# Kernel tuning notes

Hardware: AMD Instinct MI355X
Metric: run time of the kernel (lower is better)

## Reference

```python
import jax, jax.numpy as jnp
import numpy as np

B, T, C, HR = 8, 4096, 256, 4
N_LAYER, LAYER_ID = 12, 3
HID = HR * C


def _fancy_decay_first():
    # Faithful reproduction of VRWKV_SpatialMix._init_weights(init_mode='fancy')
    r01 = LAYER_ID / (N_LAYER - 1)
    h = np.arange(C, dtype=np.float32)
    decay = -5.0 + 8.0 * (h / (C - 1)) ** (0.7 + 1.3 * r01)
    zig = ((np.arange(1, C + 1) % 3) - 1).astype(np.float32) * 0.5
    first = np.float32(np.log(0.3)) + zig
    return jnp.asarray(decay, jnp.float32), jnp.asarray(first, jnp.float32)


def setup_inputs() -> dict:
    key = jax.random.key(0)
    ks = jax.random.split(key, 12)
    s = 0.02  # small weight scale keeps exp(k) well-conditioned
    decay, first = _fancy_decay_first()
    return {
        "x": jax.random.normal(ks[0], (B, T, C), jnp.float32),
        "Wk": jax.random.normal(ks[1], (C, C), jnp.float32) * s,
        "Wv": jax.random.normal(ks[2], (C, C), jnp.float32) * s,
        "Wr": jax.random.normal(ks[3], (C, C), jnp.float32) * s,
        "Wo": jax.random.normal(ks[4], (C, C), jnp.float32) * s,
        "Wk_ffn": jax.random.normal(ks[5], (C, HID), jnp.float32) * s,
        "Wv_ffn": jax.random.normal(ks[6], (HID, C), jnp.float32) * s,
        "Wr_ffn": jax.random.normal(ks[7], (C, C), jnp.float32) * s,
        "g1": 1.0 + 0.1 * jax.random.normal(ks[8], (C,), jnp.float32),
        "b1": 0.1 * jax.random.normal(ks[9], (C,), jnp.float32),
        "g2": 1.0 + 0.1 * jax.random.normal(ks[10], (C,), jnp.float32),
        "b2": 0.1 * jax.random.normal(ks[11], (C,), jnp.float32),
        "spatial_decay": decay,
        "spatial_first": first,
    }


def _ln(x, g, b):
    m = jnp.mean(x, axis=-1, keepdims=True)
    v = jnp.var(x, axis=-1, keepdims=True)
    return (x - m) * jax.lax.rsqrt(v + 1e-5) * g + b


def _wkv(w, u, k, v):
    # Numerically-stable log-space WKV recurrence (same math as wkv_cuda):
    # y_t = (sum_{i<t} e^{w*(t-1-i)+k_i} v_i + e^{u+k_t} v_t)
    #     / (sum_{i<t} e^{w*(t-1-i)+k_i}     + e^{u+k_t})
    # w,u: [C]; k,v: [B,T,C] -> y: [B,T,C]
    Bb, Tt, Cc = k.shape
    kT = jnp.swapaxes(k, 0, 1)  # [T,B,C]
    vT = jnp.swapaxes(v, 0, 1)

    def step(carry, kv):
        p, q, o = carry           # [B,C] num / den / running max exponent
        kt, vt = kv               # [B,C]
        no = jnp.maximum(o, u + kt)
        A = jnp.exp(o - no)
        E = jnp.exp(u + kt - no)
        y = (A * p + E * vt) / (A * q + E)
        no2 = jnp.maximum(w + o, kt)
        A2 = jnp.exp(w + o - no2)
        E2 = jnp.exp(kt - no2)
        return (A2 * p + E2 * vt, A2 * q + E2, no2), y

    init = (jnp.zeros((Bb, Cc), k.dtype),
            jnp.zeros((Bb, Cc), k.dtype),
            jnp.full((Bb, Cc), -1e38, k.dtype))
    _, yT = jax.lax.scan(step, init, (kT, vT))
    return jnp.swapaxes(yT, 0, 1)


def reference(x, Wk, Wv, Wr, Wo, Wk_ffn, Wv_ffn, Wr_ffn, g1, b1, g2, b2,
              spatial_decay, spatial_first):
    Tlen = x.shape[1]
    # --- SpatialMix (shift_pixel=0 -> xk=xv=xr=h, key_norm=False) ---
    h = _ln(x, g1, b1)
    k = h @ Wk
    v = h @ Wv
    sr = jax.nn.sigmoid(h @ Wr)
    y = _wkv(spatial_decay / Tlen, spatial_first / Tlen, k, v)
    x = x + (sr * y) @ Wo
    # --- ChannelMix (square-ReLU MLP, sigmoid receptance gate) ---
    h2 = _ln(x, g2, b2)
    kk = jnp.square(jax.nn.relu(h2 @ Wk_ffn))
    x = x + jax.nn.sigmoid(h2 @ Wr_ffn) * (kk @ Wv_ffn)
    return x
```

## Files before the change

### kernel.cpp

```cpp
#include <hip/hip_runtime.h>
#include <hip/hip_bf16.h>
#include <math.h>

#define TDIM 4096
#define CDIM 256
#define BDIM 8
#define NTOK (BDIM * TDIM)
#define HIDDIM 1024
#define NCHUNK 128
#define CHLEN 32

typedef float f32x4 __attribute__((ext_vector_type(4)));
typedef __bf16 bf16x8 __attribute__((ext_vector_type(8)));
typedef __bf16 bf16x4 __attribute__((ext_vector_type(4)));

#define GLDS16(gp, lp) __builtin_amdgcn_global_load_lds( \
    (const __attribute__((address_space(1))) void*)(gp), \
    (__attribute__((address_space(3))) void*)(lp), 16, 0, 0)

#define WAITCNT_VM4 0x0F74
#define WAITCNT_VM3 0x0F73
#define WAITCNT_VM0 0x0F70

__device__ __forceinline__ float sigm(float v) { return 1.0f / (1.0f + __expf(-v)); }

__global__ __launch_bounds__(256) void pack_weights(
    const float* __restrict__ Wk, const float* __restrict__ Wv,
    const float* __restrict__ Wr, const float* __restrict__ Wo,
    const float* __restrict__ Wkf, const float* __restrict__ Wvf,
    const float* __restrict__ Wrf,
    __bf16* __restrict__ WkvrT, __bf16* __restrict__ WoT,
    __bf16* __restrict__ Wkfr, __bf16* __restrict__ WvfT) {
  long long j = (long long)blockIdx.x * 256 + threadIdx.x;
  if (j < 196608) {
    int n = (int)(j >> 8), k = (int)(j & 255);
    const float* src = (n < 256) ? Wk : (n < 512 ? Wv : Wr);
    WkvrT[j] = (__bf16)src[k * 256 + (n & 255)];
    return;
  }
  j -= 196608;
  if (j < 65536) { int n = (int)(j >> 8), k = (int)(j & 255);
    WoT[j] = (__bf16)Wo[k * 256 + n]; return; }
  j -= 65536;
  if (j < 327680) { int n = (int)(j >> 8), k = (int)(j & 255);
    Wkfr[j] = (__bf16)(n < 1024 ? Wkf[(long long)k * 1024 + n]
                                : Wrf[k * 256 + (n - 1024)]);
    return; }
  j -= 327680;
  if (j < 262144) { int n = (int)(j >> 10), k = (int)(j & 1023);
    WvfT[j] = (__bf16)Wvf[(long long)k * 256 + n]; return; }
}

template <typename T>
__global__ __launch_bounds__(256) void ln_kernel(
    const T* __restrict__ x, const float* __restrict__ gamma,
    const float* __restrict__ beta, __bf16* __restrict__ h) {
  const int wave = threadIdx.x >> 6, lane = threadIdx.x & 63;
  const long long row = (long long)blockIdx.x * 4 + wave;
  const long long base = row * CDIM + lane * 4;
  f32x4 v;
  if constexpr (sizeof(T) == 4) {
    v = *(const f32x4*)&x[base];
  } else {
    bf16x4 t = *(const bf16x4*)&x[base];
    v[0] = (float)t[0]; v[1] = (float)t[1]; v[2] = (float)t[2]; v[3] = (float)t[3];
  }
  float s = v[0] + v[1] + v[2] + v[3];
  float s2 = v[0]*v[0] + v[1]*v[1] + v[2]*v[2] + v[3]*v[3];
  #pragma unroll
  for (int o = 1; o < 64; o <<= 1) { s += __shfl_xor(s, o); s2 += __shfl_xor(s2, o); }
  const float mean = s * (1.0f / CDIM);
  const float var = s2 * (1.0f / CDIM) - mean * mean;
  const float rstd = rsqrtf(var + 1e-5f);
  const f32x4 g4 = *(const f32x4*)&gamma[lane * 4];
  const f32x4 b4 = *(const f32x4*)&beta[lane * 4];
  bf16x4 o;
  #pragma unroll
  for (int r = 0; r < 4; r++) o[r] = (__bf16)((v[r] - mean) * rstd * g4[r] + b4[r]);
  *(bf16x4*)&h[base] = o;
}

template <int BN, int EPI>
__global__ __launch_bounds__(256, 5) void gemm4(
    const __bf16* __restrict__ A, const __bf16* __restrict__ Bt,
    int M, int N, int K,
    float* __restrict__ outF, __bf16* __restrict__ outH,
    __bf16* __restrict__ outH2,
    const float* __restrict__ srcF, const __bf16* __restrict__ srcH,
    const __bf16* __restrict__ gate) {
  constexpr int WNT = BN / 32;
  constexpr int NBC = BN / 64;
  __shared__ __bf16 sA[2][128 * 32];
  __shared__ __bf16 sB[2][BN * 32];

  const int tid = threadIdx.x;
  const int wave = tid >> 6, lane = tid & 63;
  const int quad = lane >> 4, mrow = lane & 15;
  const long long bm = (long long)blockIdx.x * 128;
  const long long bn = (long long)blockIdx.y * BN;
  const int wm = (wave & 1) * 64, wn = (wave >> 1) * (BN / 2);

  const int lrow = lane >> 2;
  const int lk = (lane & 3) * 8;

  auto issue = [&](int g) {
    const int buf = g & 1;
    const long long k0 = (long long)g * 32;
    const int a0 = wave * 32;
    GLDS16(A + (bm + a0 + lrow) * (long long)K + k0 + lk, &sA[buf][a0 * 32]);
    GLDS16(A + (bm + a0 + 16 + lrow) * (long long)K + k0 + lk, &sA[buf][(a0 + 16) * 32]);
    #pragma unroll
    for (int bc = 0; bc < NBC; bc++) {
      const int r0 = wave * (BN / 4) + bc * 16;
      GLDS16(Bt + (bn + r0 + lrow) * (long long)K + k0 + lk, &sB[buf][r0 * 32]);
    }
  };

  f32x4 acc[4][WNT] = {};

  const int nit = K / 32;
  issue(0);

  auto compute = [&](int i) {
    const int buf = i & 1;
    bf16x8 fa[4], fb[WNT];
    #pragma unroll
    for (int mt = 0; mt < 4; mt++)
      fa[mt] = *(const bf16x8*)&sA[buf][(wm + mt * 16 + mrow) * 32 + quad * 8];
    #pragma unroll
    for (int nt = 0; nt < WNT; nt++)
      fb[nt] = *(const bf16x8*)&sB[buf][(wn + nt * 16 + mrow) * 32 + quad * 8];
    #pragma unroll
    for (int mt = 0; mt < 4; mt++)
      #pragma unroll
      for (int nt = 0; nt < WNT; nt++)
        acc[mt][nt] = __builtin_amdgcn_mfma_f32_16x16x32_bf16(fb[nt], fa[mt], acc[mt][nt], 0, 0, 0);
  };

  #pragma unroll 1
  for (int i = 0; i < nit; i++) {
    if (i + 1 < nit) {
      issue(i + 1);
      __builtin_amdgcn_s_waitcnt(BN == 128 ? WAITCNT_VM4 : WAITCNT_VM3);
    } else {
      __builtin_amdgcn_s_waitcnt(WAITCNT_VM0);
    }
    __builtin_amdgcn_s_barrier();
    compute(i);
    if (i + 1 < nit) __builtin_amdgcn_s_barrier();
  }

  #pragma unroll
  for (int mt = 0; mt < 4; mt++) {
    #pragma unroll
    for (int nt = 0; nt < WNT; nt++) {
      const long long row = bm + wm + mt * 16 + mrow;
      const int cloc = wn + nt * 16 + quad * 4;
      const long long colb = bn + cloc;
      const f32x4 a = acc[mt][nt];
      if (EPI == 0) {
        const int plane = blockIdx.y >> 1;
        __bf16* o = outH + (long long)plane * ((long long)M * 256);
        const long long c2 = colb & 255;
        bf16x4 v;
        if (plane == 2) {
          #pragma unroll
          for (int r = 0; r < 4; r++) v[r] = (__bf16)sigm(a[r]);
        } else {
          #pragma unroll
          for (int r = 0; r < 4; r++) v[r] = (__bf16)a[r];
        }
        *(bf16x4*)&o[row * 256 + c2] = v;
      } else if (EPI == 1) {
        const long long idx = row * N + colb;
        const f32x4 s4 = *(const f32x4*)&srcF[idx];
        bf16x4 v;
        #pragma unroll
        for (int r = 0; r < 4; r++) v[r] = (__bf16)(s4[r] + a[r]);
        *(bf16x4*)&outH[idx] = v;
      } else if (EPI == 2) {
        if (blockIdx.y < 8) {
          bf16x4 v;
          #pragma unroll
          for (int r = 0; r < 4; r++) { float t = a[r] > 0.0f ? a[r] : 0.0f; v[r] = (__bf16)(t * t); }
          *(bf16x4*)&outH[row * 1024 + colb] = v;
        } else {
          bf16x4 v;
          #pragma unroll
          for (int r = 0; r < 4; r++) v[r] = (__bf16)sigm(a[r]);
          *(bf16x4*)&outH2[row * 256 + (colb - 1024)] = v;
        }
      } else {
        const long long idx = row * N + colb;
        const bf16x4 s4 = *(const bf16x4*)&srcH[idx];
        const bf16x4 g4 = *(const bf16x4*)&gate[idx];
        f32x4 v;
        #pragma unroll
        for (int r = 0; r < 4; r++) v[r] = (float)s4[r] + (float)g4[r] * a[r];
        *(f32x4*)&outF[idx] = v;
      }
    }
  }
}

__global__ __launch_bounds__(256) void wkv_phase1(
    const __bf16* __restrict__ ka, const __bf16* __restrict__ va,
    const float* __restrict__ decay,
    float* __restrict__ Sloc, float* __restrict__ Zloc) {
  const int wave = threadIdx.x >> 6, lane = threadIdx.x & 63;
  const int gi = blockIdx.x * 4 + wave;
  const int b = gi >> 7, chunk = gi & (NCHUNK - 1);
  const int c0 = lane * 4;
  const f32x4 w4 = *(const f32x4*)&decay[c0];
  f32x4 ew;
  #pragma unroll
  for (int r = 0; r < 4; r++) ew[r] = __expf(w4[r] * (1.0f / TDIM));
  f32x4 S = {0,0,0,0}, Z = {0,0,0,0};
  long long base = ((long long)b * TDIM + (long long)chunk * CHLEN) * 256 + c0;
  #pragma unroll 4
  for (int t = 0; t < CHLEN; t++) {
    const bf16x4 k4 = *(const bf16x4*)&ka[base + (long long)t * 256];
    const bf16x4 v4 = *(const bf16x4*)&va[base + (long long)t * 256];
    #pragma unroll
    for (int r = 0; r < 4; r++) {
      const float ek = __expf((float)k4[r]);
      S[r] = ew[r] * S[r] + ek * (float)v4[r];
      Z[r] = ew[r] * Z[r] + ek;
    }
  }
  const long long o = (long long)gi * 256 + c0;
  *(f32x4*)&Sloc[o] = S;
  *(f32x4*)&Zloc[o] = Z;
}

__global__ __launch_bounds__(256) void wkv_phase2(
    const float* __restrict__ Sloc, const float* __restrict__ Zloc,
    const float* __restrict__ decay,
    float* __restrict__ Sstart, float* __restrict__ Zstart) {
  const int idx = blockIdx.x * 256 + threadIdx.x;
  const int c = idx & 255;
  const int b = idx >> 8;
  const float w = decay[c] * (1.0f / TDIM);
  const float ewL = __expf(w * (float)CHLEN);
  float S = 0.0f, Z = 0.0f;
  for (int j = 0; j < NCHUNK; j++) {
    const long long o = ((long long)b * NCHUNK + j) * 256 + c;
    Sstart[o] = S;
    Zstart[o] = Z;
    S = ewL * S + Sloc[o];
    Z = ewL * Z + Zloc[o];
  }
}

__global__ __launch_bounds__(256) void wkv_phase3(
    const __bf16* __restrict__ ka, const __bf16* __restrict__ va,
    const __bf16* __restrict__ ra,
    const float* __restrict__ decay, const float* __restrict__ first,
    const float* __restrict__ Sstart, const float* __restrict__ Zstart,
    __bf16* __restrict__ a2) {
  const int wave = threadIdx.x >> 6, lane = threadIdx.x & 63;
  const int gi = blockIdx.x * 4 + wave;
  const int b = gi >> 7, chunk = gi & (NCHUNK - 1);
  const int c0 = lane * 4;
  const f32x4 w4 = *(const f32x4*)&decay[c0];
  const f32x4 u4 = *(const f32x4*)&first[c0];
  f32x4 ew, eu;
  #pragma unroll
  for (int r = 0; r < 4; r++) {
    ew[r] = __expf(w4[r] * (1.0f / TDIM));
    eu[r] = __expf(u4[r] * (1.0f / TDIM));
  }
  const long long so = (long long)gi * 256 + c0;
  f32x4 S = *(const f32x4*)&Sstart[so];
  f32x4 Z = *(const f32x4*)&Zstart[so];
  long long base = ((long long)b * TDIM + (long long)chunk * CHLEN) * 256 + c0;
  #pragma unroll 2
  for (int t = 0; t < CHLEN; t++) {
    const long long p = base + (long long)t * 256;
    const bf16x4 k4 = *(const bf16x4*)&ka[p];
    const bf16x4 v4 = *(const bf16x4*)&va[p];
    const bf16x4 r4 = *(const bf16x4*)&ra[p];
    bf16x4 o;
    #pragma unroll
    for (int r = 0; r < 4; r++) {
      const float ek = __expf((float)k4[r]);
      const float E = eu[r] * ek;
      const float y = (S[r] + E * (float)v4[r]) / (Z[r] + E);
      o[r] = (__bf16)((float)r4[r] * y);
      S[r] = ew[r] * S[r] + ek * (float)v4[r];
      Z[r] = ew[r] * Z[r] + ek;
    }
    *(bf16x4*)&a2[p] = o;
  }
}

extern "C" void kernel_launch(void* const* d_in, const int* in_sizes, int n_in,
                              void* d_out, int out_size, void* d_ws, size_t ws_size,
                              hipStream_t stream) {
  const float* x     = (const float*)d_in[0];
  const float* Wk    = (const float*)d_in[1];
  const float* Wv    = (const float*)d_in[2];
  const float* Wr    = (const float*)d_in[3];
  const float* Wo    = (const float*)d_in[4];
  const float* Wkf   = (const float*)d_in[5];
  const float* Wvf   = (const float*)d_in[6];
  const float* Wrf   = (const float*)d_in[7];
  const float* g1    = (const float*)d_in[8];
  const float* b1    = (const float*)d_in[9];
  const float* g2    = (const float*)d_in[10];
  const float* b2    = (const float*)d_in[11];
  const float* decay = (const float*)d_in[12];
  const float* first = (const float*)d_in[13];
  float* out = (float*)d_out;
  char* ws = (char*)d_ws;

  __bf16* ka     = (__bf16*)(ws + 0);
  __bf16* va     = (__bf16*)(ws + 16777216LL);
  __bf16* ra     = (__bf16*)(ws + 33554432LL);
  __bf16* a2     = (__bf16*)(ws + 50331648LL);
  __bf16* h2     = (__bf16*)(ws + 50331648LL);
  __bf16* hbuf   = (__bf16*)(ws + 67108864LL);
  __bf16* g2buf  = (__bf16*)(ws + 67108864LL);
  __bf16* x1h    = (__bf16*)(ws + 83886080LL);
  float*  Sloc   = (float*)(ws + 100663296LL);
  float*  Zloc   = (float*)(ws + 101711872LL);
  float*  Sstart = (float*)(ws + 102760448LL);
  float*  Zstart = (float*)(ws + 103809024LL);
  __bf16* kk     = (__bf16*)(ws + 100663296LL);
  __bf16* WkvrT  = (__bf16*)(ws + 167772160LL);
  __bf16* WoT    = (__bf16*)(ws + 168165376LL);
  __bf16* Wkfr   = (__bf16*)(ws + 168296448LL);
  __bf16* WvfT   = (__bf16*)(ws + 168951808LL);

  pack_weights<<<3328, 256, 0, stream>>>(Wk, Wv, Wr, Wo, Wkf, Wvf, Wrf,
                                         WkvrT, WoT, Wkfr, WvfT);

  ln_kernel<float><<<NTOK / 4, 256, 0, stream>>>(x, g1, b1, hbuf);
  gemm4<128, 0><<<dim3(NTOK / 128, 6), 256, 0, stream>>>(
      hbuf, WkvrT, NTOK, 768, CDIM, nullptr, ka, nullptr, nullptr, nullptr, nullptr);
  wkv_phase1<<<BDIM * NCHUNK / 4, 256, 0, stream>>>(ka, va, decay, Sloc, Zloc);
  wkv_phase2<<<BDIM, 256, 0, stream>>>(Sloc, Zloc, decay, Sstart, Zstart);
  wkv_phase3<<<BDIM * NCHUNK / 4, 256, 0, stream>>>(ka, va, ra, decay, first,
                                                    Sstart, Zstart, a2);
  gemm4<128, 1><<<dim3(NTOK / 128, 2), 256, 0, stream>>>(
      a2, WoT, NTOK, CDIM, CDIM, nullptr, x1h, nullptr, x, nullptr, nullptr);

  ln_kernel<__bf16><<<NTOK / 4, 256, 0, stream>>>(x1h, g2, b2, h2);
  gemm4<128, 2><<<dim3(NTOK / 128, 10), 256, 0, stream>>>(
      h2, Wkfr, NTOK, 1280, CDIM, nullptr, kk, g2buf, nullptr, nullptr, nullptr);
  gemm4<64, 3><<<dim3(NTOK / 128, 4), 256, 0, stream>>>(
      kk, WvfT, NTOK, CDIM, HIDDIM, out, nullptr, nullptr, nullptr, x1h, g2buf);
}
```

Measured before the change: 296.6 us.

## Restructure GEMMs to stream A directly into registers with B staged in swizzled LDS

Replaces the double-buffered LDS GEMM with a kernel where each wave loads its 64 rows of A straight from global memory into registers through a 3-deep prefetch ring. The B tile (64 columns by 256 of K) is staged once into LDS with an XOR swizzle to avoid bank conflicts, and is re-staged every 256 of K for the K=1024 GEMM. Tiles become 256x64 and K is a template parameter, so the loop is fully unrolled. This removes the per-iteration barriers and A traffic through LDS, at the cost of more registers (occupancy hint lowered to 3) and uncoalesced 16-byte A loads per lane.

```diff
diff --git a/kernel.cpp b/kernel.cpp
--- a/kernel.cpp
+++ b/kernel.cpp
@@ -17,10 +17,6 @@
 #define GLDS16(gp, lp) __builtin_amdgcn_global_load_lds( \
     (const __attribute__((address_space(1))) void*)(gp), \
     (__attribute__((address_space(3))) void*)(lp), 16, 0, 0)
-
-#define WAITCNT_VM4 0x0F74
-#define WAITCNT_VM3 0x0F73
-#define WAITCNT_VM0 0x0F70
 
 __device__ __forceinline__ float sigm(float v) { return 1.0f / (1.0f + __expf(-v)); }
 
@@ -80,86 +76,88 @@
   *(bf16x4*)&h[base] = o;
 }
 
-template <int BN, int EPI>
-__global__ __launch_bounds__(256, 5) void gemm4(
+template <int K, int EPI>
+__global__ __launch_bounds__(256, 3) void gemm5(
     const __bf16* __restrict__ A, const __bf16* __restrict__ Bt,
-    int M, int N, int K,
+    int M, int N,
     float* __restrict__ outF, __bf16* __restrict__ outH,
     __bf16* __restrict__ outH2,
     const float* __restrict__ srcF, const __bf16* __restrict__ srcH,
     const __bf16* __restrict__ gate) {
-  constexpr int WNT = BN / 32;
-  constexpr int NBC = BN / 64;
-  __shared__ __bf16 sA[2][128 * 32];
-  __shared__ __bf16 sB[2][BN * 32];
+  constexpr int NIT = K / 32;
+  __shared__ __bf16 sB[64 * 256];
 
   const int tid = threadIdx.x;
   const int wave = tid >> 6, lane = tid & 63;
   const int quad = lane >> 4, mrow = lane & 15;
-  const long long bm = (long long)blockIdx.x * 128;
-  const long long bn = (long long)blockIdx.y * BN;
-  const int wm = (wave & 1) * 64, wn = (wave >> 1) * (BN / 2);
-
-  const int lrow = lane >> 2;
-  const int lk = (lane & 3) * 8;
-
-  auto issue = [&](int g) {
-    const int buf = g & 1;
-    const long long k0 = (long long)g * 32;
-    const int a0 = wave * 32;
-    GLDS16(A + (bm + a0 + lrow) * (long long)K + k0 + lk, &sA[buf][a0 * 32]);
-    GLDS16(A + (bm + a0 + 16 + lrow) * (long long)K + k0 + lk, &sA[buf][(a0 + 16) * 32]);
-    #pragma unroll
-    for (int bc = 0; bc < NBC; bc++) {
-      const int r0 = wave * (BN / 4) + bc * 16;
-      GLDS16(Bt + (bn + r0 + lrow) * (long long)K + k0 + lk, &sB[buf][r0 * 32]);
+  const long long m0 = (long long)blockIdx.x * 256 + wave * 64;
+  const long long bn = (long long)blockIdx.y * 64;
+
+  auto stageB = [&](int c) {
+    #pragma unroll
+    for (int i = 0; i < 8; i++) {
+      const int j = i * 256 + tid;
+      const int row = j >> 5;
+      const int kc = ((j & 31) ^ (row & 31)) * 8;
+      GLDS16(Bt + (bn + row) * (long long)K + c * 256 + kc,
+             &sB[(i * 256 + wave * 64) * 8]);
     }
   };
 
-  f32x4 acc[4][WNT] = {};
-
-  const int nit = K / 32;
-  issue(0);
-
-  auto compute = [&](int i) {
-    const int buf = i & 1;
-    bf16x8 fa[4], fb[WNT];
+  const __bf16* pA[4];
+  #pragma unroll
+  for (int mt = 0; mt < 4; mt++)
+    pA[mt] = A + (m0 + mt * 16 + mrow) * (long long)K + quad * 8;
+
+  f32x4 acc[4][4] = {};
+  bf16x8 fa[3][4];
+
+  stageB(0);
+  __syncthreads();
+
+  auto loadA = [&](int i, int s) {
     #pragma unroll
     for (int mt = 0; mt < 4; mt++)
-      fa[mt] = *(const bf16x8*)&sA[buf][(wm + mt * 16 + mrow) * 32 + quad * 8];
-    #pragma unroll
-    for (int nt = 0; nt < WNT; nt++)
-      fb[nt] = *(const bf16x8*)&sB[buf][(wn + nt * 16 + mrow) * 32 + quad * 8];
+      fa[s][mt] = *(const bf16x8*)(pA[mt] + (long long)i * 32);
+  };
+  loadA(0, 0);
+  if (NIT > 1) loadA(1, 1);
+
+  #pragma unroll
+  for (int i = 0; i < NIT; i++) {
+    if constexpr (K > 256) {
+      if ((i & 7) == 0 && i > 0) {
+        __syncthreads();
+        stageB(i >> 3);
+        __syncthreads();
+      }
+    }
+    if (i + 2 < NIT) loadA(i + 2, (i + 2) % 3);
+    const int ii = i & 7;
+    bf16x8 fb[4];
+    #pragma unroll
+    for (int nt = 0; nt < 4; nt++) {
+      const int n = nt * 16 + mrow;
+      const int pos = (ii * 4 + quad) ^ (n & 31);
+      fb[nt] = *(const bf16x8*)&sB[n * 256 + pos * 8];
+    }
     #pragma unroll
     for (int mt = 0; mt < 4; mt++)
       #pragma unroll
-      for (int nt = 0; nt < WNT; nt++)
-        acc[mt][nt] = __builtin_amdgcn_mfma_f32_16x16x32_bf16(fb[nt], fa[mt], acc[mt][nt], 0, 0, 0);
-  };
-
-  #pragma unroll 1
-  for (int i = 0; i < nit; i++) {
-    if (i + 1 < nit) {
-      issue(i + 1);
-      __builtin_amdgcn_s_waitcnt(BN == 128 ? WAITCNT_VM4 : WAITCNT_VM3);
-    } else {
-      __builtin_amdgcn_s_waitcnt(WAITCNT_VM0);
-    }
-    __builtin_amdgcn_s_barrier();
-    compute(i);
-    if (i + 1 < nit) __builtin_amdgcn_s_barrier();
+      for (int nt = 0; nt < 4; nt++)
+        acc[mt][nt] = __builtin_amdgcn_mfma_f32_16x16x32_bf16(fb[nt], fa[i % 3][mt], acc[mt][nt], 0, 0, 0);
   }
 
   #pragma unroll
   for (int mt = 0; mt < 4; mt++) {
     #pragma unroll
-    for (int nt = 0; nt < WNT; nt++) {
-      const long long row = bm + wm + mt * 16 + mrow;
-      const int cloc = wn + nt * 16 + quad * 4;
+    for (int nt = 0; nt < 4; nt++) {
+      const long long row = m0 + mt * 16 + mrow;
+      const int cloc = nt * 16 + quad * 4;
       const long long colb = bn + cloc;
       const f32x4 a = acc[mt][nt];
       if (EPI == 0) {
-        const int plane = blockIdx.y >> 1;
+        const int plane = blockIdx.y >> 2;
         __bf16* o = outH + (long long)plane * ((long long)M * 256);
         const long long c2 = colb & 255;
         bf16x4 v;
@@ -179,7 +177,7 @@
         for (int r = 0; r < 4; r++) v[r] = (__bf16)(s4[r] + a[r]);
         *(bf16x4*)&outH[idx] = v;
       } else if (EPI == 2) {
-        if (blockIdx.y < 8) {
+        if (blockIdx.y < 16) {
           bf16x4 v;
           #pragma unroll
           for (int r = 0; r < 4; r++) { float t = a[r] > 0.0f ? a[r] : 0.0f; v[r] = (__bf16)(t * t); }
@@ -336,18 +334,18 @@
                                          WkvrT, WoT, Wkfr, WvfT);
 
   ln_kernel<float><<<NTOK / 4, 256, 0, stream>>>(x, g1, b1, hbuf);
-  gemm4<128, 0><<<dim3(NTOK / 128, 6), 256, 0, stream>>>(
-      hbuf, WkvrT, NTOK, 768, CDIM, nullptr, ka, nullptr, nullptr, nullptr, nullptr);
+  gemm5<256, 0><<<dim3(NTOK / 256, 12), 256, 0, stream>>>(
+      hbuf, WkvrT, NTOK, 768, nullptr, ka, nullptr, nullptr, nullptr, nullptr);
   wkv_phase1<<<BDIM * NCHUNK / 4, 256, 0, stream>>>(ka, va, decay, Sloc, Zloc);
   wkv_phase2<<<BDIM, 256, 0, stream>>>(Sloc, Zloc, decay, Sstart, Zstart);
   wkv_phase3<<<BDIM * NCHUNK / 4, 256, 0, stream>>>(ka, va, ra, decay, first,
                                                     Sstart, Zstart, a2);
-  gemm4<128, 1><<<dim3(NTOK / 128, 2), 256, 0, stream>>>(
-      a2, WoT, NTOK, CDIM, CDIM, nullptr, x1h, nullptr, x, nullptr, nullptr);
+  gemm5<256, 1><<<dim3(NTOK / 256, 4), 256, 0, stream>>>(
+      a2, WoT, NTOK, 256, nullptr, x1h, nullptr, x, nullptr, nullptr);
 
   ln_kernel<__bf16><<<NTOK / 4, 256, 0, stream>>>(x1h, g2, b2, h2);
-  gemm4<128, 2><<<dim3(NTOK / 128, 10), 256, 0, stream>>>(
-      h2, Wkfr, NTOK, 1280, CDIM, nullptr, kk, g2buf, nullptr, nullptr, nullptr);
-  gemm4<64, 3><<<dim3(NTOK / 128, 4), 256, 0, stream>>>(
-      kk, WvfT, NTOK, CDIM, HIDDIM, out, nullptr, nullptr, nullptr, x1h, g2buf);
-}
+  gemm5<256, 2><<<dim3(NTOK / 256, 20), 256, 0, stream>>>(
+      h2, Wkfr, NTOK, 1280, nullptr, kk, g2buf, nullptr, nullptr, nullptr);
+  gemm5<1024, 3><<<dim3(NTOK / 256, 4), 256, 0, stream>>>(
+      kk, WvfT, NTOK, 256, out, nullptr, nullptr, nullptr, x1h, g2buf);
+}
```

Result: slower. 324.1 us (+9.3%).
